# Performance work log

Hardware: AMD Instinct MI355X
Metric: run time of the kernel (lower is better)

Reference implementation:

```python
import jax, jax.numpy as jnp
import numpy as np

K = 3            # kernel_size
FILTERS = 256
GC = 16          # group_channels (hardcoded in module)
G = FILTERS // GC  # groups = 16


def setup_inputs() -> dict:
    key = jax.random.key(0)
    ks = jax.random.split(key, 5)
    B, H, W, C = 8, 64, 64, FILTERS
    red = FILTERS // 4  # reduction_ratio = 4
    x = jax.random.normal(ks[0], (B, H, W, C), dtype=jnp.float32)
    W1 = jax.random.normal(ks[1], (C, red), dtype=jnp.float32) * 0.05
    b1 = jnp.zeros((red,), dtype=jnp.float32)
    W2 = jax.random.normal(ks[2], (red, K * K * G), dtype=jnp.float32) * 0.05
    b2 = jnp.zeros((K * K * G,), dtype=jnp.float32)
    return {"x": x, "W1": W1, "b1": b1, "W2": W2, "b2": b2}


def reference(x, W1, b1, W2, b2):
    b, h, w, c = x.shape
    kk = K * K
    # kernel generator: two 1x1 convs (note: norm1/relu1 are defined but unused in the original call())
    wgt = jnp.einsum('bhwc,cd->bhwd', x, W1) + b1          # [b,h,w,c/4]
    wgt = jnp.einsum('bhwd,de->bhwe', wgt, W2) + b2        # [b,h,w,kk*G]
    # transpose to channel-first, reshape (b, G, kk, h, w), expand group-channel dim
    wgt = wgt.transpose(0, 3, 1, 2).reshape(b, G, 1, kk, h, w)
    # SAME-padded 3x3 patch extraction, stride 1; TF depth layout is (ki, kj, c)
    pad = (K - 1) // 2
    xp = jnp.pad(x, ((0, 0), (pad, K - 1 - pad), (pad, K - 1 - pad), (0, 0)))
    patches = jnp.stack([xp[:, i:i + h, j:j + w, :] for i in range(K) for j in range(K)], axis=3)  # [b,h,w,kk,c]
    # replicate TF's transpose + row-major reshape of the (kk*c) flat dim into (G, GC, kk)
    out = patches.reshape(b, h, w, kk * c).transpose(0, 3, 1, 2).reshape(b, G, GC, kk, h, w)
    out = jnp.einsum('bgokhw,bgckhw->bgchw', wgt, out)     # multiply + reduce over kk
    out = out.reshape(b, FILTERS, h, w).transpose(0, 2, 3, 1)
    return out
```

## Files before the change

kernel.cpp:

```cpp
#include <hip/hip_runtime.h>

namespace {
constexpr int XP = 264;
constexpr int XR = 18 * XP;
constexpr int EWP = 148;

typedef _Float16 h2 __attribute__((ext_vector_type(2)));
typedef _Float16 h8 __attribute__((ext_vector_type(8)));
typedef float f32x4 __attribute__((ext_vector_type(4)));

__device__ __forceinline__ h2 pkrtz(float a, float b) {
  return __builtin_bit_cast(h2, __builtin_amdgcn_cvt_pkrtz(a, b));
}

#if __has_builtin(__builtin_amdgcn_fdot2)
#define HAS_FDOT2 1
#else
#define HAS_FDOT2 0
#endif

__global__ __launch_bounds__(256) void prep_w12(
    const float* __restrict__ W1, const float* __restrict__ b1,
    const float* __restrict__ W2, const float* __restrict__ b2,
    _Float16* __restrict__ pack, float* __restrict__ b12)
{
  const int t = threadIdx.x;
  const int T = blockIdx.x;
  if (T < 9) {
    __shared__ float sw2[64 * 16];
    for (int i = t; i < 1024; i += 256) {
      int d = i >> 4, n = i & 15;
      sw2[i] = W2[d * 144 + T * 16 + n];
    }
    __syncthreads();
    const int c = t;
    float acc[16];
#pragma unroll
    for (int n = 0; n < 16; ++n) acc[n] = 0.f;
    for (int d = 0; d < 64; d += 4) {
      float4 w1 = *(const float4*)(W1 + c * 64 + d);
#pragma unroll
      for (int dd = 0; dd < 4; ++dd) {
        float a = (dd == 0) ? w1.x : (dd == 1) ? w1.y : (dd == 2) ? w1.z : w1.w;
        const float* r = &sw2[(d + dd) * 16];
#pragma unroll
        for (int n = 0; n < 16; ++n) acc[n] += a * r[n];
      }
    }
    int s = c >> 5, q = (c >> 3) & 3, j = c & 7;
#pragma unroll
    for (int n = 0; n < 16; ++n)
      pack[(((T * 8 + s) * 64 + q * 16 + n) << 3) + j] = (_Float16)acc[n];
  } else if (t < 144) {
    float bb = b2[t];
    for (int d = 0; d < 64; ++d) bb += b1[d] * W2[d * 144 + t];
    b12[t] = bb;
  }
}

__global__ __launch_bounds__(256, 4) void invo_fused(
    const float* __restrict__ x,
    const _Float16* __restrict__ pack,
    const float* __restrict__ b12g,
    float* __restrict__ out)
{
  __shared__ __align__(16) _Float16 xg[3 * XR];
  __shared__ float ew[16 * EWP];

  const int t = threadIdx.x;
  const int blk = blockIdx.x;
  const int b = blk & 7;
  const int r_ = blk >> 3;
  const int strip = r_ & 3;
  const int h = r_ >> 2;
  const int w0 = strip * 16;
  const int pix0 = ((b << 6) + h) * 64 + w0;
  const int wave = t >> 6, lane = t & 63;

  h8 Bpre[8];
  {
    const h8* bp = (const h8*)pack + (wave * 8) * 64 + lane;
#pragma unroll
    for (int s = 0; s < 8; ++s) Bpre[s] = bp[s * 64];
  }

  {
    float4 va[7][2];
    int dst[7];
    bool ok[7];
#pragma unroll
    for (int i = 0; i < 7; ++i) {
      int idx = i * 256 + t;
      ok[i] = idx < 1728;
      int cc = idx & 31;
      int pj = idx >> 5;
      int r = (pj >= 36) ? 2 : (pj >= 18 ? 1 : 0);
      int j = pj - r * 18;
      int hh = h + r - 1, ww = w0 + j - 1;
      dst[i] = r * XR + j * XP + cc * 8;
      va[i][0] = make_float4(0.f, 0.f, 0.f, 0.f);
      va[i][1] = make_float4(0.f, 0.f, 0.f, 0.f);
      if (ok[i] && ((unsigned)hh < 64u) && ((unsigned)ww < 64u)) {
        const float* src = x + ((((b << 6) + hh) << 6) + ww) * 256 + cc * 8;
        va[i][0] = *(const float4*)(src);
        va[i][1] = *(const float4*)(src + 4);
      }
    }
#pragma unroll
    for (int i = 0; i < 7; ++i) {
      if (ok[i]) {
        uint4 o;
        o.x = __builtin_bit_cast(unsigned, pkrtz(va[i][0].x, va[i][0].y));
        o.y = __builtin_bit_cast(unsigned, pkrtz(va[i][0].z, va[i][0].w));
        o.z = __builtin_bit_cast(unsigned, pkrtz(va[i][1].x, va[i][1].y));
        o.w = __builtin_bit_cast(unsigned, pkrtz(va[i][1].z, va[i][1].w));
        *(uint4*)(&xg[dst[i]]) = o;
      }
    }
  }
  __syncthreads();

  {
    const int q = lane >> 4, m = lane & 15;
    h8 A[8];
    const _Float16* arow = &xg[XR + (m + 1) * XP + q * 8];
#pragma unroll
    for (int s = 0; s < 8; ++s)
      A[s] = *(const h8*)(arow + s * 32);
    {
      const int T = wave;
      f32x4 acc = {0.f, 0.f, 0.f, 0.f};
#pragma unroll
      for (int s = 0; s < 8; ++s)
        acc = __builtin_amdgcn_mfma_f32_16x16x32_f16(A[s], Bpre[s], acc, 0, 0, 0);
      float bb = b12g[T * 16 + m];
#pragma unroll
      for (int r = 0; r < 4; ++r)
        ew[(q * 4 + r) * EWP + T * 16 + m] = acc[r] + bb;
    }
    for (int T = wave + 4; T < 9; T += 4) {
      f32x4 acc = {0.f, 0.f, 0.f, 0.f};
      const h8* bp = (const h8*)pack + (T * 8) * 64 + lane;
#pragma unroll
      for (int s = 0; s < 8; ++s)
        acc = __builtin_amdgcn_mfma_f32_16x16x32_f16(A[s], bp[s * 64], acc, 0, 0, 0);
      float bb = b12g[T * 16 + m];
#pragma unroll
      for (int r = 0; r < 4; ++r)
        ew[(q * 4 + r) * EWP + T * 16 + m] = acc[r] + bb;
    }
  }
  __syncthreads();

  {
    const int p = t >> 4, g = t & 15;
    float ewr[9];
#pragma unroll
    for (int k = 0; k < 9; ++k) ewr[k] = ew[p * EWP + g * 9 + k];
    h2 wp[8];
#pragma unroll
    for (int m = 0; m < 8; ++m)
      wp[m] = pkrtz(ewr[m], ewr[m + 1]);
    const float w8 = ewr[8], wb0 = ewr[0];
    const int g144 = g * 144;
    const int pbase = p * XP;
    float res[16];
#pragma unroll
    for (int gc = 0; gc < 16; ++gc) res[gc] = 0.f;
#pragma unroll
    for (int j = 0; j < 18; ++j) {
      int f = g144 + j * 8;
      int tap = f >> 8;
      int ch = f & 255;
      int di = (tap * 86) >> 8;
      int off = XP * (tap + 15 * di) + ch;
      uint4 dv = *(const uint4*)(&xg[pbase + off]);
      h2 v[4];
      v[0] = __builtin_bit_cast(h2, dv.x);
      v[1] = __builtin_bit_cast(h2, dv.y);
      v[2] = __builtin_bit_cast(h2, dv.z);
      v[3] = __builtin_bit_cast(h2, dv.w);
#pragma unroll
      for (int i = 0; i < 4; ++i) {
        const int u = j * 8 + 2 * i;
        const int m = u % 9;
        if (m == 8) {
          res[u / 9]     += (float)v[i][0] * w8;
          res[u / 9 + 1] += (float)v[i][1] * wb0;
        } else {
#if HAS_FDOT2
          res[u / 9] = __builtin_amdgcn_fdot2(v[i], wp[m], res[u / 9], false);
#else
          res[u / 9] += (float)v[i][0] * ewr[m] + (float)v[i][1] * ewr[m + 1];
#endif
        }
      }
    }
    float* orow = out + (size_t)(pix0 + p) * 256 + (g << 4);
    *(float4*)(orow + 0)  = make_float4(res[0],  res[1],  res[2],  res[3]);
    *(float4*)(orow + 4)  = make_float4(res[4],  res[5],  res[6],  res[7]);
    *(float4*)(orow + 8)  = make_float4(res[8],  res[9],  res[10], res[11]);
    *(float4*)(orow + 12) = make_float4(res[12], res[13], res[14], res[15]);
  }
}
}

extern "C" void kernel_launch(void* const* d_in, const int* in_sizes, int n_in,
                              void* d_out, int out_size, void* d_ws, size_t ws_size,
                              hipStream_t stream) {
  const float* x  = (const float*)d_in[0];
  const float* W1 = (const float*)d_in[1];
  const float* b1 = (const float*)d_in[2];
  const float* W2 = (const float*)d_in[3];
  const float* b2 = (const float*)d_in[4];
  float* out = (float*)d_out;
  _Float16* pack = (_Float16*)d_ws;
  float* b12 = (float*)((char*)d_ws + 73728);
  prep_w12<<<10, 256, 0, stream>>>(W1, b1, W2, b2, pack, b12);
  invo_fused<<<2048, 256, 0, stream>>>(x, pack, b12, out);
}
```

Baseline: 110.7 us.

## Process two output rows per 512-thread block to reuse halo rows

Each block now covers two output rows of a 16-pixel strip with 512 threads, staging four input rows in LDS instead of three per single row. This cuts redundant halo loads and fp16 conversion of x, and halves the grid. All eight waves compute kernel-weight tiles 0-7 for both rows, and waves 0-1 handle tile 8. Output stores become nontemporal. LDS use grows to about 57KB per block, which may limit how many blocks fit on a CU.

Measured after the change: 117.6 us. +6.2%, slower.

```diff
diff --git a/kernel.cpp b/kernel.cpp
--- a/kernel.cpp
+++ b/kernel.cpp
@@ -58,23 +58,23 @@
   }
 }
 
-__global__ __launch_bounds__(256, 4) void invo_fused(
+__global__ __launch_bounds__(512, 4) void invo_fused(
     const float* __restrict__ x,
     const _Float16* __restrict__ pack,
     const float* __restrict__ b12g,
     float* __restrict__ out)
 {
-  __shared__ __align__(16) _Float16 xg[3 * XR];
-  __shared__ float ew[16 * EWP];
+  __shared__ __align__(16) _Float16 xg[4 * XR];
+  __shared__ float ew[32 * EWP];
 
   const int t = threadIdx.x;
   const int blk = blockIdx.x;
   const int b = blk & 7;
   const int r_ = blk >> 3;
   const int strip = r_ & 3;
-  const int h = r_ >> 2;
-  const int w0 = strip * 16;
-  const int pix0 = ((b << 6) + h) * 64 + w0;
+  const int hp = r_ >> 2;
+  const int h = hp << 1;
+  const int w0 = strip << 4;
   const int wave = t >> 6, lane = t & 63;
 
   h8 Bpre[8];
@@ -85,16 +85,16 @@
   }
 
   {
-    float4 va[7][2];
-    int dst[7];
-    bool ok[7];
-#pragma unroll
-    for (int i = 0; i < 7; ++i) {
-      int idx = i * 256 + t;
-      ok[i] = idx < 1728;
+    float4 va[5][2];
+    int dst[5];
+    bool ok[5];
+#pragma unroll
+    for (int i = 0; i < 5; ++i) {
+      int idx = i * 512 + t;
+      ok[i] = idx < 2304;
       int cc = idx & 31;
       int pj = idx >> 5;
-      int r = (pj >= 36) ? 2 : (pj >= 18 ? 1 : 0);
+      int r = (pj >= 54) ? 3 : (pj >= 36) ? 2 : (pj >= 18) ? 1 : 0;
       int j = pj - r * 18;
       int hh = h + r - 1, ww = w0 + j - 1;
       dst[i] = r * XR + j * XP + cc * 8;
@@ -107,7 +107,7 @@
       }
     }
 #pragma unroll
-    for (int i = 0; i < 7; ++i) {
+    for (int i = 0; i < 5; ++i) {
       if (ok[i]) {
         uint4 o;
         o.x = __builtin_bit_cast(unsigned, pkrtz(va[i][0].x, va[i][0].y));
@@ -123,37 +123,53 @@
   {
     const int q = lane >> 4, m = lane & 15;
     h8 A[8];
-    const _Float16* arow = &xg[XR + (m + 1) * XP + q * 8];
-#pragma unroll
-    for (int s = 0; s < 8; ++s)
-      A[s] = *(const h8*)(arow + s * 32);
+    const _Float16* a0 = &xg[XR + (m + 1) * XP + q * 8];
+#pragma unroll
+    for (int s = 0; s < 8; ++s) A[s] = *(const h8*)(a0 + s * 32);
     {
-      const int T = wave;
       f32x4 acc = {0.f, 0.f, 0.f, 0.f};
 #pragma unroll
       for (int s = 0; s < 8; ++s)
         acc = __builtin_amdgcn_mfma_f32_16x16x32_f16(A[s], Bpre[s], acc, 0, 0, 0);
-      float bb = b12g[T * 16 + m];
+      float bb = b12g[wave * 16 + m];
 #pragma unroll
       for (int r = 0; r < 4; ++r)
-        ew[(q * 4 + r) * EWP + T * 16 + m] = acc[r] + bb;
-    }
-    for (int T = wave + 4; T < 9; T += 4) {
+        ew[(q * 4 + r) * EWP + wave * 16 + m] = acc[r] + bb;
+    }
+#pragma unroll
+    for (int s = 0; s < 8; ++s) A[s] = *(const h8*)(a0 + XR + s * 32);
+    {
       f32x4 acc = {0.f, 0.f, 0.f, 0.f};
-      const h8* bp = (const h8*)pack + (T * 8) * 64 + lane;
 #pragma unroll
       for (int s = 0; s < 8; ++s)
-        acc = __builtin_amdgcn_mfma_f32_16x16x32_f16(A[s], bp[s * 64], acc, 0, 0, 0);
-      float bb = b12g[T * 16 + m];
+        acc = __builtin_amdgcn_mfma_f32_16x16x32_f16(A[s], Bpre[s], acc, 0, 0, 0);
+      float bb = b12g[wave * 16 + m];
 #pragma unroll
       for (int r = 0; r < 4; ++r)
-        ew[(q * 4 + r) * EWP + T * 16 + m] = acc[r] + bb;
+        ew[(16 + q * 4 + r) * EWP + wave * 16 + m] = acc[r] + bb;
+    }
+    if (wave < 2) {
+      const _Float16* ar = a0 + (wave ? XR : 0);
+#pragma unroll
+      for (int s = 0; s < 8; ++s) A[s] = *(const h8*)(ar + s * 32);
+      const h8* bp = (const h8*)pack + 64 * 64 + lane;
+#pragma unroll
+      for (int s = 0; s < 8; ++s) Bpre[s] = bp[s * 64];
+      f32x4 acc = {0.f, 0.f, 0.f, 0.f};
+#pragma unroll
+      for (int s = 0; s < 8; ++s)
+        acc = __builtin_amdgcn_mfma_f32_16x16x32_f16(A[s], Bpre[s], acc, 0, 0, 0);
+      float bb = b12g[128 + m];
+#pragma unroll
+      for (int r = 0; r < 4; ++r)
+        ew[(wave * 16 + q * 4 + r) * EWP + 128 + m] = acc[r] + bb;
     }
   }
   __syncthreads();
 
   {
     const int p = t >> 4, g = t & 15;
+    const int hi = p >> 4, pl = p & 15;
     float ewr[9];
 #pragma unroll
     for (int k = 0; k < 9; ++k) ewr[k] = ew[p * EWP + g * 9 + k];
@@ -163,7 +179,7 @@
       wp[m] = pkrtz(ewr[m], ewr[m + 1]);
     const float w8 = ewr[8], wb0 = ewr[0];
     const int g144 = g * 144;
-    const int pbase = p * XP;
+    const int pbase = hi * XR + pl * XP;
     float res[16];
 #pragma unroll
     for (int gc = 0; gc < 16; ++gc) res[gc] = 0.f;
@@ -196,11 +212,15 @@
         }
       }
     }
-    float* orow = out + (size_t)(pix0 + p) * 256 + (g << 4);
-    *(float4*)(orow + 0)  = make_float4(res[0],  res[1],  res[2],  res[3]);
-    *(float4*)(orow + 4)  = make_float4(res[4],  res[5],  res[6],  res[7]);
-    *(float4*)(orow + 8)  = make_float4(res[8],  res[9],  res[10], res[11]);
-    *(float4*)(orow + 12) = make_float4(res[12], res[13], res[14], res[15]);
+    float* orow = out + (size_t)((((b << 6) + h + hi) << 6) + w0 + pl) * 256 + (g << 4);
+    f32x4 o0 = {res[0],  res[1],  res[2],  res[3]};
+    f32x4 o1 = {res[4],  res[5],  res[6],  res[7]};
+    f32x4 o2 = {res[8],  res[9],  res[10], res[11]};
+    f32x4 o3 = {res[12], res[13], res[14], res[15]};
+    __builtin_nontemporal_store(o0, (f32x4*)(orow + 0));
+    __builtin_nontemporal_store(o1, (f32x4*)(orow + 4));
+    __builtin_nontemporal_store(o2, (f32x4*)(orow + 8));
+    __builtin_nontemporal_store(o3, (f32x4*)(orow + 12));
   }
 }
 }
@@ -217,5 +237,5 @@
   _Float16* pack = (_Float16*)d_ws;
   float* b12 = (float*)((char*)d_ws + 73728);
   prep_w12<<<10, 256, 0, stream>>>(W1, b1, W2, b2, pack, b12);
-  invo_fused<<<2048, 256, 0, stream>>>(x, pack, b12, out);
-}
+  invo_fused<<<1024, 512, 0, stream>>>(x, pack, b12, out);
+}
```
